# Performance work log

Hardware: AMD Instinct MI355X
Metric: run time of the kernel (lower is better)

Reference implementation:

```python
import jax, jax.numpy as jnp
import numpy as np

NEG = -1000000.0

def setup_inputs() -> dict:
    key = jax.random.key(0)
    k1, k2, k3, k4 = jax.random.split(key, 4)
    B, S, D = 32, 2048, 64  # batch_eff=batch*heads, seq_len, head_dim
    queries = jax.random.normal(k1, (B, S, D), dtype=jnp.float32)
    keys = jax.random.normal(k2, (B, S, D), dtype=jnp.float32)
    values = jax.random.normal(k3, (B, S, D), dtype=jnp.float32)
    valid_len = jax.random.randint(k4, (B,), 1, S + 1, dtype=jnp.int32)
    return {"queries": queries, "keys": keys, "values": values, "valid_len": valid_len}

def reference(queries, keys, values, valid_len):
    # scores: (B, Sq, Sk) = QK^T / sqrt(d)
    d = queries.shape[-1]
    scores = jnp.einsum('bqd,bkd->bqk', queries, keys) / jnp.sqrt(jnp.float32(d))
    # padding mask from per-batch valid key lengths: True where position is padded
    k_len = keys.shape[1]
    pad_mask = jnp.arange(k_len)[None, None, :] >= valid_len[:, None, None]  # (B,1,Sk)
    scores = jnp.where(pad_mask, NEG, scores)
    attn = jax.nn.softmax(scores, axis=-1)
    # dropout is identity in eval / reference mode
    return jnp.einsum('bqk,bkd->bqd', attn, values)
```

## Files before the change

kernel.cpp:

```cpp
#include <hip/hip_runtime.h>

typedef unsigned short ushort_t;
typedef short short8 __attribute__((ext_vector_type(8)));
typedef float f32x4 __attribute__((ext_vector_type(4)));
typedef unsigned int u32x4 __attribute__((ext_vector_type(4)));

typedef f32x4 f32x4a __attribute__((may_alias));
typedef u32x4 u32x4a __attribute__((may_alias));
typedef short8 short8a __attribute__((may_alias));

#define BC 64
#define PRP 74

#define BAR_LGKM() asm volatile("s_waitcnt lgkmcnt(0)\n\ts_barrier" ::: "memory")
#define BAR_VM4()  asm volatile("s_waitcnt vmcnt(4)\n\ts_barrier" ::: "memory")
#define BAR_VM0()  asm volatile("s_waitcnt vmcnt(0)\n\ts_barrier" ::: "memory")

__device__ __forceinline__ ushort_t f2bf(float x) {
    unsigned u = __float_as_uint(x);
    u = (u + 0x7fffu + ((u >> 16) & 1u)) >> 16;
    return (ushort_t)u;
}

__device__ __forceinline__ void dma16(const void* g, void* lds) {
    __builtin_amdgcn_global_load_lds(
        (const __attribute__((address_space(1))) unsigned int*)g,
        (__attribute__((address_space(3))) unsigned int*)lds, 16, 0, 0);
}

__global__ __launch_bounds__(256) void prep_kv(
    const float* __restrict__ K, const float* __restrict__ V,
    ushort_t* __restrict__ Kb, ushort_t* __restrict__ Vt, int S, int jtiles)
{
    __shared__ ushort_t T[64 * 66];
    const int b  = blockIdx.x / jtiles;
    const int j0 = (blockIdx.x % jtiles) * 64;
    const int tid = threadIdx.x;

    {
        const int jj = tid >> 2, d0 = (tid & 3) * 16;
        const float* src = K + ((size_t)b * S + j0 + jj) * 64 + d0;
        f32x4 k0 = *(const f32x4a*)(src),     k1 = *(const f32x4a*)(src + 4);
        f32x4 k2 = *(const f32x4a*)(src + 8), k3 = *(const f32x4a*)(src + 12);
        u32x4 w0, w1;
#pragma unroll
        for (int k = 0; k < 2; ++k) {
            w0[k]   = (unsigned)f2bf(k0[2*k]) | ((unsigned)f2bf(k0[2*k+1]) << 16);
            w0[k+2] = (unsigned)f2bf(k1[2*k]) | ((unsigned)f2bf(k1[2*k+1]) << 16);
            w1[k]   = (unsigned)f2bf(k2[2*k]) | ((unsigned)f2bf(k2[2*k+1]) << 16);
            w1[k+2] = (unsigned)f2bf(k3[2*k]) | ((unsigned)f2bf(k3[2*k+1]) << 16);
        }
        ushort_t* dst = Kb + ((size_t)b * S + j0 + jj) * 64 + d0;
        *(u32x4a*)dst = w0;
        *(u32x4a*)(dst + 8) = w1;
    }

    {
        const float* Vb = V + ((size_t)b * S + j0) * 64;
#pragma unroll
        for (int p = 0; p < 4; ++p) {
            int jj = p * 16 + (tid >> 4), d4 = (tid & 15) * 4;
            f32x4 v = *(const f32x4a*)(Vb + (size_t)jj * 64 + d4);
#pragma unroll
            for (int k = 0; k < 4; ++k) T[(d4 + k) * 66 + jj] = f2bf(v[k]);
        }
        __syncthreads();
        const int d = tid >> 2, j16 = (tid & 3) * 16;
        ushort_t* dst = Vt + ((size_t)b * 64 + d) * S + j0 + j16;
        u32x4 w0, w1;
#pragma unroll
        for (int k = 0; k < 4; ++k) {
            w0[k] = (unsigned)T[d*66 + j16 + 2*k]     | ((unsigned)T[d*66 + j16 + 2*k + 1] << 16);
            w1[k] = (unsigned)T[d*66 + j16 + 8 + 2*k] | ((unsigned)T[d*66 + j16 + 9 + 2*k] << 16);
        }
        *(u32x4a*)dst = w0;
        *(u32x4a*)(dst + 8) = w1;
    }
}

__global__ __launch_bounds__(256, 4) void attn_persist(
    const float* __restrict__ Q, const ushort_t* __restrict__ Kb,
    const ushort_t* __restrict__ Vt, const int* __restrict__ VL,
    float* __restrict__ O, int* __restrict__ cnt,
    int NB, int S, int qtiles, int nitems)
{
    __shared__ __align__(16) ushort_t Kbuf[2][64 * 64];
    __shared__ __align__(16) ushort_t Vbuf[2][64 * 64];
    __shared__ int order_s[64];
    __shared__ int item_s;

    const int tid  = threadIdx.x;
    const int wave = tid >> 6;
    const int lane = tid & 63;
    const int qd   = lane >> 4;
    const int c    = lane & 15;
    const int q8   = qd * 8;

    if (tid < NB && NB <= 64) {
        const int myL = VL[tid];
        int rank = 0;
        for (int j = 0; j < NB; ++j) {
            const int Lj = VL[j];
            rank += (Lj > myL) || (Lj == myL && j < tid);
        }
        order_s[rank] = tid;
    }
    __syncthreads();

    const int r0 = wave * 16 + (lane >> 3);
    const int r1 = r0 + 8;
    const int bdp = lane & 7;
    const int swz0 = ((bdp - r0) & 7) * 16;
    const int swz1 = ((bdp - r1) & 7) * 16;
    const int ldsoff0 = wave * 1024;
    const int ldsoff1 = ldsoff0 + 512;

    const int pr0 = ((r0 >> 4) & 1) * 32 + ((r0 >> 2) & 3) * 8 + ((r0 >> 5) & 1) * 4 + (r0 & 3);
    const int pr1 = ((r1 >> 4) & 1) * 32 + ((r1 >> 2) & 3) * 8 + ((r1 >> 5) & 1) * 4 + (r1 & 3);

    int off[2][4];
#pragma unroll
    for (int x = 0; x < 2; ++x)
#pragma unroll
        for (int y = 0; y < 4; ++y) {
            const int row = y * 16 + c;
            off[x][y] = row * 128 + (((x * 4 + qd) + row) & 7) * 16;
        }

    const float qs = 0.125f * 1.4426950408889634f;
    const f32x4 zero4 = {0.0f, 0.0f, 0.0f, 0.0f};

    for (;;) {
        if (tid == 0) item_s = atomicAdd(cnt, 1);
        __syncthreads();
        const int it = item_s;
        if (it >= nitems) break;

        const int b  = order_s[it / qtiles];
        const int qt = it % qtiles;
        const int qrow0 = qt * 64 + wave * 16;
        const int L   = VL[b];
        const int nkt = (L + BC - 1) / BC;

        short8 qf[2];
        {
            const float* Qb = Q + ((size_t)b * S + qrow0) * 64;
#pragma unroll
            for (int kc = 0; kc < 2; ++kc) {
                const float* qp = Qb + c * 64 + kc * 32 + q8;
                f32x4 a = *(const f32x4a*)qp;
                f32x4 bq = *(const f32x4a*)(qp + 4);
                short8 f;
#pragma unroll
                for (int k = 0; k < 4; ++k) {
                    f[k]   = (short)f2bf(a[k] * qs);
                    f[k+4] = (short)f2bf(bq[k] * qs);
                }
                qf[kc] = f;
            }
        }

        f32x4 oacc[4];
#pragma unroll
        for (int dt = 0; dt < 4; ++dt) oacc[dt] = zero4;
        float rs0 = 0.0f, rs1 = 0.0f;

        const char* KbB = (const char*)(Kb + (size_t)b * S * 64);
        const char* VtB = (const char*)(Vt + (size_t)b * 64 * S);
        const char* kg0 = KbB + pr0 * 128 + swz0;
        const char* kg1 = KbB + pr1 * 128 + swz1;
        const char* vg0 = VtB + (size_t)r0 * (S * 2) + swz0;
        const char* vg1 = VtB + (size_t)r1 * (S * 2) + swz1;

        dma16(kg0, Kbuf[0] + ldsoff0);
        dma16(kg1, Kbuf[0] + ldsoff1);
        dma16(vg0, Vbuf[0] + ldsoff0);
        dma16(vg1, Vbuf[0] + ldsoff1);

        for (int kt = 0; kt < nkt; ++kt) {
            const int j0 = kt * BC;
            const ushort_t* Kt  = Kbuf[kt & 1];
            const ushort_t* Vb_ = Vbuf[kt & 1];

            if (kt + 1 < nkt) {
                const size_t ko = (size_t)(kt + 1) * 8192;
                const size_t vo = (size_t)(kt + 1) * 128;
                ushort_t* kb = Kbuf[(kt + 1) & 1];
                ushort_t* vb = Vbuf[(kt + 1) & 1];
                dma16(kg0 + ko, kb + ldsoff0);
                dma16(kg1 + ko, kb + ldsoff1);
                dma16(vg0 + vo, vb + ldsoff0);
                dma16(vg1 + vo, vb + ldsoff1);
                BAR_VM4();
            } else {
                BAR_VM0();
            }

            f32x4 sacc[4];
#pragma unroll
            for (int nt = 0; nt < 4; ++nt) sacc[nt] = zero4;
#pragma unroll
            for (int kc = 0; kc < 2; ++kc) {
#pragma unroll
                for (int nt = 0; nt < 4; ++nt) {
                    short8 kf = *(const short8a*)((const char*)Kt + off[kc][nt]);
                    sacc[nt] = __builtin_amdgcn_mfma_f32_16x16x32_bf16(kf, qf[kc], sacc[nt], 0, 0, 0);
                }
            }

            const int lim = L - j0 - q8;
            float p[4][4];
#pragma unroll
            for (int nt = 0; nt < 4; ++nt) {
                const int kb2 = (nt & 1) * 32 + ((nt >> 1) << 2);
#pragma unroll
                for (int r = 0; r < 4; ++r) {
                    const bool valid = (kb2 + r < lim);
                    const float e = valid ? exp2f(sacc[nt][r]) : 0.0f;
                    p[nt][r] = e;
                    if (nt & 1) rs1 += e; else rs0 += e;
                }
            }

#pragma unroll
            for (int jc = 0; jc < 2; ++jc) {
                u32x4 w;
                w[0] = (unsigned)f2bf(p[jc][0])     | ((unsigned)f2bf(p[jc][1])     << 16);
                w[1] = (unsigned)f2bf(p[jc][2])     | ((unsigned)f2bf(p[jc][3])     << 16);
                w[2] = (unsigned)f2bf(p[jc + 2][0]) | ((unsigned)f2bf(p[jc + 2][1]) << 16);
                w[3] = (unsigned)f2bf(p[jc + 2][2]) | ((unsigned)f2bf(p[jc + 2][3]) << 16);
                const short8 pf = __builtin_bit_cast(short8, w);
#pragma unroll
                for (int dt = 0; dt < 4; ++dt) {
                    short8 vf = *(const short8a*)((const char*)Vb_ + off[jc][dt]);
                    oacc[dt] = __builtin_amdgcn_mfma_f32_16x16x32_bf16(pf, vf, oacc[dt], 0, 0, 0);
                }
            }

            BAR_LGKM();
        }

        float rsum = rs0 + rs1;
        rsum += __shfl_xor(rsum, 16);
        rsum += __shfl_xor(rsum, 32);
        const float inv = 1.0f / rsum;
#pragma unroll
        for (int r = 0; r < 4; ++r) {
            const float invr = __shfl(inv, (lane & 48) | (qd * 4 + r));
            const int row = qrow0 + qd * 4 + r;
            float* dst = O + ((size_t)b * S + row) * 64;
#pragma unroll
            for (int dt = 0; dt < 4; ++dt)
                dst[dt * 16 + c] = oacc[dt][r] * invr;
        }
    }
}

__global__ __launch_bounds__(256, 4) void attn_mono(
    const float* __restrict__ Q, const float* __restrict__ K,
    const float* __restrict__ V, const int* __restrict__ VL,
    float* __restrict__ O, int NB, int S)
{
    __shared__ ushort_t Ksh[BC * PRP];
    __shared__ ushort_t Vsh[64 * PRP];
    __shared__ ushort_t Psh[4 * 16 * PRP];
    const int tid = threadIdx.x, wave = tid >> 6, lane = tid & 63;
    const int qd = lane >> 4, c = lane & 15, q8 = qd * 8;
    const int bid = blockIdx.x;
    const int b = (bid & 7) | (((bid >> 3) & 3) << 3);
    const int qt = bid >> 5;
    const int qrow0 = qt * 64 + wave * 16;
    const int L = VL[b];
    const int nkt = (L + BC - 1) / BC;
    const size_t bbase = (size_t)b * S * 64;
    const int kj = tid >> 2, kd = (tid & 3) * 16;
    const int vp = tid & 31, vd = (tid >> 5) * 8;
    const float qs = 0.125f * 1.4426950408889634f;
    short8 qf[2];
    {
        const float* Qb = Q + bbase + (size_t)qrow0 * 64;
#pragma unroll
        for (int kc = 0; kc < 2; ++kc) {
            const float* p = Qb + c * 64 + kc * 32 + q8;
            f32x4 a = *(const f32x4a*)p;
            f32x4 bq = *(const f32x4a*)(p + 4);
            short8 f;
#pragma unroll
            for (int k = 0; k < 4; ++k) { f[k] = (short)f2bf(a[k]*qs); f[k+4] = (short)f2bf(bq[k]*qs); }
            qf[kc] = f;
        }
    }
    const f32x4 zero4 = {0.0f, 0.0f, 0.0f, 0.0f};
    f32x4 oacc[4];
#pragma unroll
    for (int dt = 0; dt < 4; ++dt) oacc[dt] = zero4;
    float lrow[4] = {0, 0, 0, 0};
    ushort_t* Pw = Psh + wave * (16 * PRP);
    for (int kt = 0; kt < nkt; ++kt) {
        const int j0 = kt * BC;
        __syncthreads();
        {
            const float* src = K + bbase + (size_t)(j0 + kj) * 64 + kd;
            f32x4 k0 = *(const f32x4a*)(src), k1 = *(const f32x4a*)(src + 4);
            f32x4 k2 = *(const f32x4a*)(src + 8), k3 = *(const f32x4a*)(src + 12);
            u32x4 w0, w1;
#pragma unroll
            for (int k = 0; k < 2; ++k) {
                w0[k]   = (unsigned)f2bf(k0[2*k]) | ((unsigned)f2bf(k0[2*k+1]) << 16);
                w0[k+2] = (unsigned)f2bf(k1[2*k]) | ((unsigned)f2bf(k1[2*k+1]) << 16);
                w1[k]   = (unsigned)f2bf(k2[2*k]) | ((unsigned)f2bf(k2[2*k+1]) << 16);
                w1[k+2] = (unsigned)f2bf(k3[2*k]) | ((unsigned)f2bf(k3[2*k+1]) << 16);
            }
            *(u32x4a*)&Ksh[kj * PRP + kd] = w0;
            *(u32x4a*)&Ksh[kj * PRP + kd + 8] = w1;
        }
        {
            const float* src = V + bbase + (size_t)(j0 + 2 * vp) * 64 + vd;
            f32x4 a0 = *(const f32x4a*)(src), a1 = *(const f32x4a*)(src + 4);
            f32x4 b0 = *(const f32x4a*)(src + 64), b1 = *(const f32x4a*)(src + 68);
#pragma unroll
            for (int kk = 0; kk < 8; ++kk) {
                float av = (kk < 4) ? a0[kk & 3] : a1[kk & 3];
                float bv = (kk < 4) ? b0[kk & 3] : b1[kk & 3];
                *(unsigned __attribute__((may_alias))*)&Vsh[(vd + kk) * PRP + 2 * vp] =
                    (unsigned)f2bf(av) | ((unsigned)f2bf(bv) << 16);
            }
        }
        __syncthreads();
        f32x4 sacc[4];
#pragma unroll
        for (int nt = 0; nt < 4; ++nt) sacc[nt] = zero4;
#pragma unroll
        for (int kc = 0; kc < 2; ++kc)
#pragma unroll
            for (int nt = 0; nt < 4; ++nt) {
                short8 kf = *(const short8a*)&Ksh[(nt * 16 + c) * PRP + kc * 32 + q8];
                sacc[nt] = __builtin_amdgcn_mfma_f32_16x16x32_bf16(qf[kc], kf, sacc[nt], 0, 0, 0);
            }
#pragma unroll
        for (int nt = 0; nt < 4; ++nt) {
            const bool valid = (j0 + nt * 16 + c) < L;
#pragma unroll
            for (int r = 0; r < 4; ++r) {
                float p = valid ? exp2f(sacc[nt][r]) : 0.0f;
                lrow[r] += p;
                Pw[(qd * 4 + r) * PRP + nt * 16 + c] = f2bf(p);
            }
        }
#pragma unroll
        for (int jc = 0; jc < 2; ++jc) {
            short8 pf = *(const short8a*)&Pw[c * PRP + jc * 32 + q8];
#pragma unroll
            for (int dt = 0; dt < 4; ++dt) {
                short8 vf = *(const short8a*)&Vsh[(dt * 16 + c) * PRP + jc * 32 + q8];
                oacc[dt] = __builtin_amdgcn_mfma_f32_16x16x32_bf16(pf, vf, oacc[dt], 0, 0, 0);
            }
        }
    }
#pragma unroll
    for (int r = 0; r < 4; ++r) {
        float ls = lrow[r];
        ls += __shfl_xor(ls, 1); ls += __shfl_xor(ls, 2);
        ls += __shfl_xor(ls, 4); ls += __shfl_xor(ls, 8);
        const float inv = 1.0f / ls;
        const int row = qrow0 + qd * 4 + r;
        float* dst = O + bbase + (size_t)row * 64;
#pragma unroll
        for (int dt = 0; dt < 4; ++dt) dst[dt * 16 + c] = oacc[dt][r] * inv;
    }
}

extern "C" void kernel_launch(void* const* d_in, const int* in_sizes, int n_in,
                              void* d_out, int out_size, void* d_ws, size_t ws_size,
                              hipStream_t stream) {
    const float* Q = (const float*)d_in[0];
    const float* K = (const float*)d_in[1];
    const float* V = (const float*)d_in[2];
    const int*  VL = (const int*)d_in[3];
    float*      Op = (float*)d_out;

    const int NB = in_sizes[3];
    const int S  = in_sizes[0] / (NB * 64);
    const int qtiles = S / 64;
    const int jtiles = S / 64;
    const size_t nelem = (size_t)NB * S * 64;
    const size_t bf_bytes = nelem * 2;

    if (ws_size >= 256 + 2 * bf_bytes && NB <= 64) {
        int* cnt = (int*)d_ws;
        ushort_t* Kb = (ushort_t*)((char*)d_ws + 256);
        ushort_t* Vt = (ushort_t*)((char*)d_ws + 256 + bf_bytes);
        hipMemsetAsync(d_ws, 0, 256, stream);
        prep_kv<<<dim3(NB * jtiles), dim3(256), 0, stream>>>(K, V, Kb, Vt, S, jtiles);
        const int nitems = NB * qtiles;
        const int grid = nitems < 1024 ? nitems : 1024;
        attn_persist<<<dim3(grid), dim3(256), 0, stream>>>(
            Q, Kb, Vt, VL, Op, cnt, NB, S, qtiles, nitems);
    } else {
        attn_mono<<<dim3(NB * qtiles), dim3(256), 0, stream>>>(Q, K, V, VL, Op, NB, S);
    }
}
```

Measured before the change: 169.4 us.

## Triple-buffer K/V tiles, store V transposed per tile, add MFMA priority hints

The prep kernel now writes transposed V as contiguous 64x64 tiles, so each V tile is one contiguous 8KB block addressed like K. The attention kernel moves to a three-stage LDS ring that prefetches two tiles ahead, and it issues those loads before converting Q to hide more global-memory latency. It also raises wave priority around the MFMA blocks. The extra LDS per block lowers the launch-bounds occupancy target from 4 to 3 and shrinks the persistent grid from 1024 to 768, which may reduce latency hiding across waves.

```diff
diff --git a/kernel.cpp b/kernel.cpp
--- a/kernel.cpp
+++ b/kernel.cpp
@@ -13,6 +13,7 @@
 #define PRP 74
 
 #define BAR_LGKM() asm volatile("s_waitcnt lgkmcnt(0)\n\ts_barrier" ::: "memory")
+#define BAR_VM8()  asm volatile("s_waitcnt vmcnt(8)\n\ts_barrier" ::: "memory")
 #define BAR_VM4()  asm volatile("s_waitcnt vmcnt(4)\n\ts_barrier" ::: "memory")
 #define BAR_VM0()  asm volatile("s_waitcnt vmcnt(0)\n\ts_barrier" ::: "memory")
 
@@ -34,7 +35,8 @@
 {
     __shared__ ushort_t T[64 * 66];
     const int b  = blockIdx.x / jtiles;
-    const int j0 = (blockIdx.x % jtiles) * 64;
+    const int jt = blockIdx.x % jtiles;
+    const int j0 = jt * 64;
     const int tid = threadIdx.x;
 
     {
@@ -66,7 +68,7 @@
         }
         __syncthreads();
         const int d = tid >> 2, j16 = (tid & 3) * 16;
-        ushort_t* dst = Vt + ((size_t)b * 64 + d) * S + j0 + j16;
+        ushort_t* dst = Vt + ((size_t)(b * jtiles + jt)) * 4096 + d * 64 + j16;
         u32x4 w0, w1;
 #pragma unroll
         for (int k = 0; k < 4; ++k) {
@@ -78,14 +80,14 @@
     }
 }
 
-__global__ __launch_bounds__(256, 4) void attn_persist(
+__global__ __launch_bounds__(256, 3) void attn_persist(
     const float* __restrict__ Q, const ushort_t* __restrict__ Kb,
     const ushort_t* __restrict__ Vt, const int* __restrict__ VL,
     float* __restrict__ O, int* __restrict__ cnt,
     int NB, int S, int qtiles, int nitems)
 {
-    __shared__ __align__(16) ushort_t Kbuf[2][64 * 64];
-    __shared__ __align__(16) ushort_t Vbuf[2][64 * 64];
+    __shared__ __align__(16) ushort_t Kbuf[3][64 * 64];
+    __shared__ __align__(16) ushort_t Vbuf[3][64 * 64];
     __shared__ int order_s[64];
     __shared__ int item_s;
 
@@ -142,6 +144,24 @@
         const int L   = VL[b];
         const int nkt = (L + BC - 1) / BC;
 
+        const char* KbB = (const char*)(Kb + (size_t)b * S * 64);
+        const char* VtB = (const char*)(Vt + (size_t)b * S * 64);
+        const char* kg0 = KbB + pr0 * 128 + swz0;
+        const char* kg1 = KbB + pr1 * 128 + swz1;
+        const char* vg0 = VtB + r0 * 128 + swz0;
+        const char* vg1 = VtB + r1 * 128 + swz1;
+
+        dma16(kg0, Kbuf[0] + ldsoff0);
+        dma16(kg1, Kbuf[0] + ldsoff1);
+        dma16(vg0, Vbuf[0] + ldsoff0);
+        dma16(vg1, Vbuf[0] + ldsoff1);
+        if (nkt > 1) {
+            dma16(kg0 + 8192, Kbuf[1] + ldsoff0);
+            dma16(kg1 + 8192, Kbuf[1] + ldsoff1);
+            dma16(vg0 + 8192, Vbuf[1] + ldsoff0);
+            dma16(vg1 + 8192, Vbuf[1] + ldsoff1);
+        }
+
         short8 qf[2];
         {
             const float* Qb = Q + ((size_t)b * S + qrow0) * 64;
@@ -165,32 +185,21 @@
         for (int dt = 0; dt < 4; ++dt) oacc[dt] = zero4;
         float rs0 = 0.0f, rs1 = 0.0f;
 
-        const char* KbB = (const char*)(Kb + (size_t)b * S * 64);
-        const char* VtB = (const char*)(Vt + (size_t)b * 64 * S);
-        const char* kg0 = KbB + pr0 * 128 + swz0;
-        const char* kg1 = KbB + pr1 * 128 + swz1;
-        const char* vg0 = VtB + (size_t)r0 * (S * 2) + swz0;
-        const char* vg1 = VtB + (size_t)r1 * (S * 2) + swz1;
-
-        dma16(kg0, Kbuf[0] + ldsoff0);
-        dma16(kg1, Kbuf[0] + ldsoff1);
-        dma16(vg0, Vbuf[0] + ldsoff0);
-        dma16(vg1, Vbuf[0] + ldsoff1);
-
+        int cur = 0;
         for (int kt = 0; kt < nkt; ++kt) {
             const int j0 = kt * BC;
-            const ushort_t* Kt  = Kbuf[kt & 1];
-            const ushort_t* Vb_ = Vbuf[kt & 1];
-
-            if (kt + 1 < nkt) {
-                const size_t ko = (size_t)(kt + 1) * 8192;
-                const size_t vo = (size_t)(kt + 1) * 128;
-                ushort_t* kb = Kbuf[(kt + 1) & 1];
-                ushort_t* vb = Vbuf[(kt + 1) & 1];
-                dma16(kg0 + ko, kb + ldsoff0);
-                dma16(kg1 + ko, kb + ldsoff1);
-                dma16(vg0 + vo, vb + ldsoff0);
-                dma16(vg1 + vo, vb + ldsoff1);
+            const ushort_t* Kt  = Kbuf[cur];
+            const ushort_t* Vb_ = Vbuf[cur];
+
+            if (kt + 2 < nkt) {
+                const int pre = (cur == 0) ? 2 : cur - 1;
+                const size_t ko = (size_t)(kt + 2) * 8192;
+                dma16(kg0 + ko, Kbuf[pre] + ldsoff0);
+                dma16(kg1 + ko, Kbuf[pre] + ldsoff1);
+                dma16(vg0 + ko, Vbuf[pre] + ldsoff0);
+                dma16(vg1 + ko, Vbuf[pre] + ldsoff1);
+                BAR_VM8();
+            } else if (kt + 1 < nkt) {
                 BAR_VM4();
             } else {
                 BAR_VM0();
@@ -199,6 +208,7 @@
             f32x4 sacc[4];
 #pragma unroll
             for (int nt = 0; nt < 4; ++nt) sacc[nt] = zero4;
+            __builtin_amdgcn_s_setprio(1);
 #pragma unroll
             for (int kc = 0; kc < 2; ++kc) {
 #pragma unroll
@@ -207,6 +217,7 @@
                     sacc[nt] = __builtin_amdgcn_mfma_f32_16x16x32_bf16(kf, qf[kc], sacc[nt], 0, 0, 0);
                 }
             }
+            __builtin_amdgcn_s_setprio(0);
 
             const int lim = L - j0 - q8;
             float p[4][4];
@@ -222,6 +233,7 @@
                 }
             }
 
+            __builtin_amdgcn_s_setprio(1);
 #pragma unroll
             for (int jc = 0; jc < 2; ++jc) {
                 u32x4 w;
@@ -236,8 +248,10 @@
                     oacc[dt] = __builtin_amdgcn_mfma_f32_16x16x32_bf16(pf, vf, oacc[dt], 0, 0, 0);
                 }
             }
+            __builtin_amdgcn_s_setprio(0);
 
             BAR_LGKM();
+            cur = (cur == 2) ? 0 : cur + 1;
         }
 
         float rsum = rs0 + rs1;
@@ -393,7 +407,7 @@
         hipMemsetAsync(d_ws, 0, 256, stream);
         prep_kv<<<dim3(NB * jtiles), dim3(256), 0, stream>>>(K, V, Kb, Vt, S, jtiles);
         const int nitems = NB * qtiles;
-        const int grid = nitems < 1024 ? nitems : 1024;
+        const int grid = nitems < 768 ? nitems : 768;
         attn_persist<<<dim3(grid), dim3(256), 0, stream>>>(
             Q, Kb, Vt, VL, Op, cnt, NB, S, qtiles, nitems);
     } else {
```

After: 155.3 us. -8.3%, faster.
